# Kernel tuning notes

Hardware: AMD Instinct MI355X
Metric: run time of the kernel (lower is better)

The kernel has to match this reference:

```python
import jax, jax.numpy as jnp
import numpy as np

B, T, D = 64, 2048, 512
UNITS = 10  # hardcoded in original module


def setup_inputs() -> dict:
    key = jax.random.key(0)
    ks = jax.random.split(key, 6)
    Eo = jax.random.normal(ks[0], (B, T, D), dtype=jnp.float32)
    H = jax.random.normal(ks[1], (B, D), dtype=jnp.float32)
    # Keras Dense params: kernel [in, out], bias [out] (glorot-ish scale)
    W_eo = jax.random.normal(ks[2], (D, UNITS), dtype=jnp.float32) * (1.0 / np.sqrt(D))
    b_eo = jnp.zeros((UNITS,), dtype=jnp.float32)
    W_h = jax.random.normal(ks[3], (D, UNITS), dtype=jnp.float32) * (1.0 / np.sqrt(D))
    b_h = jnp.zeros((UNITS,), dtype=jnp.float32)
    W_s = jax.random.normal(ks[4], (UNITS, 1), dtype=jnp.float32) * (1.0 / np.sqrt(UNITS))
    b_s = jnp.zeros((1,), dtype=jnp.float32)
    return {"Eo": Eo, "H": H, "W_eo": W_eo, "b_eo": b_eo,
            "W_h": W_h, "b_h": b_h, "W_s": W_s, "b_s": b_s}


def reference(Eo, H, W_eo, b_eo, W_h, b_h, W_s, b_s):
    # Eo: [B, T, D], H: [B, D]
    Eo_d = jnp.einsum('btd,du->btu', Eo, W_eo) + b_eo          # [B, T, U]
    H_d = H @ W_h + b_h                                        # [B, U]
    EoH = jnp.tanh(Eo_d + H_d[:, None, :])                     # [B, T, U]
    score = jnp.einsum('btu,uo->bto', EoH, W_s) + b_s          # [B, T, 1]
    weight = jax.nn.softmax(score, axis=1)                     # softmax over T
    context = jnp.sum(Eo * weight, axis=1)                     # [B, D]
    return (context, weight)
```

## Files before the change

### kernel.cpp

```cpp
#include <hip/hip_runtime.h>
#include <math.h>

#define BB 64
#define TT 2048
#define DD 512
#define UU 10
#define S_CHUNKS 16
#define CHUNK_T (TT / S_CHUNKS)
#define NB (CHUNK_T / 16)

__device__ __forceinline__ float fast_tanh(float x) {
    return 1.0f - 2.0f / (1.0f + __expf(2.0f * x));
}

template<int K>
__device__ __forceinline__ float dpp_shr(float x) {
    int xi = __builtin_bit_cast(int, x);
    int r  = __builtin_amdgcn_update_dpp(0, xi, 0x110 | K, 0xF, 0xF, true);
    return __builtin_bit_cast(float, r);
}

__device__ __forceinline__ float read_lane_f(float v, int lane) {
    return __builtin_bit_cast(float,
        __builtin_amdgcn_readlane(__builtin_bit_cast(int, v), lane));
}

typedef __attribute__((address_space(1))) const void gvoid;
typedef __attribute__((address_space(3))) void lvoid;
__device__ __forceinline__ void dma16(const float* g, float* l) {
    __builtin_amdgcn_global_load_lds((gvoid*)g, (lvoid*)l, 16, 0, 0);
}

__global__ __launch_bounds__(256) void attn_pass1(
    const float* __restrict__ Eo, const float* __restrict__ H,
    const float* __restrict__ W_eo, const float* __restrict__ b_eo,
    const float* __restrict__ W_h, const float* __restrict__ b_h,
    const float* __restrict__ W_s, const float* __restrict__ b_s,
    float* __restrict__ pexp, float* __restrict__ pc)
{
    const int b     = blockIdx.y;
    const int chunk = blockIdx.x;
    const int tid   = threadIdx.x;
    const int wave  = tid >> 6;
    const int lane  = tid & 63;

    __shared__ __align__(16) float buf[4][2][4][DD];
    __shared__ float sc[4][DD];

    float hacc[UU];
    #pragma unroll
    for (int u = 0; u < UU; ++u) hacc[u] = 0.f;
    const float* Hb = H + (size_t)b * DD;
    #pragma unroll
    for (int k = 0; k < DD / 64; ++k) {
        float hv = Hb[k * 64 + lane];
        const float* wr = W_h + (size_t)(k * 64 + lane) * UU;
        #pragma unroll
        for (int u = 0; u < UU; ++u) hacc[u] += hv * wr[u];
    }
    #pragma unroll
    for (int off = 1; off < 64; off <<= 1) {
        #pragma unroll
        for (int u = 0; u < UU; ++u) hacc[u] += __shfl_xor(hacc[u], off, 64);
    }
    float hb[UU];
    #pragma unroll
    for (int u = 0; u < UU; ++u) hb[u] = hacc[u] + b_h[u] + b_eo[u];

    float wsv[UU];
    #pragma unroll
    for (int u = 0; u < UU; ++u) wsv[u] = W_s[u];
    const float bs = b_s[0];

    float wv[8][UU];
    #pragma unroll
    for (int k = 0; k < 2; ++k) {
        #pragma unroll
        for (int j = 0; j < 4; ++j) {
            const float* wr = W_eo + (size_t)(k * 256 + 4 * lane + j) * UU;
            #pragma unroll
            for (int u = 0; u < UU; ++u) wv[k * 4 + j][u] = wr[u];
        }
    }

    float l = 0.f;
    float c[8];
    #pragma unroll
    for (int j = 0; j < 8; ++j) c[j] = 0.f;

    const int  t0w  = chunk * CHUNK_T + wave * (CHUNK_T / 4);
    const bool lo32 = (lane & 32) == 0;
    const bool lo16 = (lane & 16) == 0;
    const float* rowb = Eo + (size_t)b * TT * DD + 4 * lane;

    #pragma unroll
    for (int tt = 0; tt < 4; ++tt) {
        const float* g = rowb + (size_t)(t0w + tt) * DD;
        dma16(g,       &buf[wave][0][tt][0]);
        dma16(g + 256, &buf[wave][0][tt][256]);
    }

    auto do_batch = [&](int i) {
        const int cur = i & 1, nxt = cur ^ 1;
        if (i + 1 < NB) {
            #pragma unroll
            for (int tt = 0; tt < 4; ++tt) {
                const float* g = rowb + (size_t)(t0w + (i + 1) * 4 + tt) * DD;
                dma16(g,       &buf[wave][nxt][tt][0]);
                dma16(g + 256, &buf[wave][nxt][tt][256]);
            }
        }
        __builtin_amdgcn_sched_barrier(0);

        const int tb = t0w + i * 4;
        float e[4][8];
        #pragma unroll
        for (int tt = 0; tt < 4; ++tt) {
            float4 e0 = *(const float4*)&buf[wave][cur][tt][4 * lane];
            float4 e1 = *(const float4*)&buf[wave][cur][tt][256 + 4 * lane];
            e[tt][0] = e0.x; e[tt][1] = e0.y; e[tt][2] = e0.z; e[tt][3] = e0.w;
            e[tt][4] = e1.x; e[tt][5] = e1.y; e[tt][6] = e1.z; e[tt][7] = e1.w;
        }

        float acc[4][UU];
        #pragma unroll
        for (int tt = 0; tt < 4; ++tt) {
            #pragma unroll
            for (int u = 0; u < UU; ++u) acc[tt][u] = 0.f;
            #pragma unroll
            for (int j = 0; j < 8; ++j) {
                #pragma unroll
                for (int u = 0; u < UU; ++u) acc[tt][u] += e[tt][j] * wv[j][u];
            }
        }

        float s = bs;
        #pragma unroll
        for (int u = 0; u < UU; ++u) {
            float y0 = lo32 ? acc[0][u] : acc[2][u];
            float o0 = lo32 ? acc[2][u] : acc[0][u];
            y0 += __shfl_xor(o0, 32, 64);
            float y1 = lo32 ? acc[1][u] : acc[3][u];
            float o1 = lo32 ? acc[3][u] : acc[1][u];
            y1 += __shfl_xor(o1, 32, 64);
            float z  = lo16 ? y0 : y1;
            float oz = lo16 ? y1 : y0;
            z += __shfl_xor(oz, 16, 64);
            z += dpp_shr<1>(z);
            z += dpp_shr<2>(z);
            z += dpp_shr<4>(z);
            z += dpp_shr<8>(z);
            s += wsv[u] * fast_tanh(z + hb[u]);
        }
        float p = __expf(s);

        if ((lane & 15) == 15) pexp[(size_t)b * TT + tb + (lane >> 4)] = p;

        float p0 = read_lane_f(p, 15);
        float p1 = read_lane_f(p, 31);
        float p2 = read_lane_f(p, 47);
        float p3 = read_lane_f(p, 63);
        l += (p0 + p1) + (p2 + p3);
        #pragma unroll
        for (int j = 0; j < 8; ++j)
            c[j] += p0 * e[0][j] + p1 * e[1][j] + p2 * e[2][j] + p3 * e[3][j];
    };

    asm volatile("s_waitcnt vmcnt(0)" ::: "memory");
    __builtin_amdgcn_sched_barrier(0);
    do_batch(0);
    for (int i = 1; i < NB; ++i) {
        asm volatile("s_waitcnt vmcnt(1)" ::: "memory");
        __builtin_amdgcn_sched_barrier(0);
        do_batch(i);
    }

    #pragma unroll
    for (int k = 0; k < 2; ++k) {
        #pragma unroll
        for (int j = 0; j < 4; ++j)
            sc[wave][k * 256 + 4 * lane + j] = c[k * 4 + j];
    }
    __syncthreads();

    const int pidx = b * S_CHUNKS + chunk;
    for (int d = tid; d < DD; d += 256) {
        pc[(size_t)pidx * DD + d] = (sc[0][d] + sc[1][d]) + (sc[2][d] + sc[3][d]);
    }
}

__global__ __launch_bounds__(256) void attn_epilogue(
    const float* __restrict__ pexp, const float* __restrict__ pc,
    float* __restrict__ ctx_out, float* __restrict__ wout)
{
    const int b    = blockIdx.x >> 2;
    const int part = blockIdx.x & 3;
    const int tid  = threadIdx.x;
    const int wave = tid >> 6;

    float s = 0.f;
    #pragma unroll
    for (int k = 0; k < TT / 256; ++k) s += pexp[(size_t)b * TT + k * 256 + tid];
    #pragma unroll
    for (int off = 1; off < 64; off <<= 1) s += __shfl_xor(s, off, 64);

    __shared__ float sl[4];
    if ((tid & 63) == 0) sl[wave] = s;
    __syncthreads();
    const float l = (sl[0] + sl[1]) + (sl[2] + sl[3]);
    const float inv = 1.0f / l;

    const int d = part * (DD / 4) + tid;
    if (tid < DD / 4) {
        float v = 0.f;
        #pragma unroll
        for (int sss = 0; sss < S_CHUNKS; ++sss)
            v += pc[((size_t)(b * S_CHUNKS + sss)) * DD + d];
        ctx_out[(size_t)b * DD + d] = v * inv;
    }
    #pragma unroll
    for (int k = 0; k < 2; ++k) {
        const int t = part * (TT / 4) + k * 256 + tid;
        wout[(size_t)b * TT + t] = pexp[(size_t)b * TT + t] * inv;
    }
}

extern "C" void kernel_launch(void* const* d_in, const int* in_sizes, int n_in,
                              void* d_out, int out_size, void* d_ws, size_t ws_size,
                              hipStream_t stream) {
    const float* Eo   = (const float*)d_in[0];
    const float* H    = (const float*)d_in[1];
    const float* W_eo = (const float*)d_in[2];
    const float* b_eo = (const float*)d_in[3];
    const float* W_h  = (const float*)d_in[4];
    const float* b_h  = (const float*)d_in[5];
    const float* W_s  = (const float*)d_in[6];
    const float* b_s  = (const float*)d_in[7];

    float* pexp = (float*)d_ws;
    float* pc   = pexp + (size_t)BB * TT;

    float* out_ctx = (float*)d_out;
    float* out_w   = out_ctx + (size_t)BB * DD;

    dim3 gridA(S_CHUNKS, BB);
    attn_pass1<<<gridA, 256, 0, stream>>>(Eo, H, W_eo, b_eo, W_h, b_h, W_s, b_s,
                                          pexp, pc);
    attn_epilogue<<<BB * 4, 256, 0, stream>>>(pexp, pc, out_ctx, out_w);
}
```

Before: 65.32 us.

## Fuse epilogue into main kernel via last-block atomic counter

```diff
diff --git a/kernel.cpp b/kernel.cpp
--- a/kernel.cpp
+++ b/kernel.cpp
@@ -31,12 +31,18 @@
     __builtin_amdgcn_global_load_lds((gvoid*)g, (lvoid*)l, 16, 0, 0);
 }
 
-__global__ __launch_bounds__(256) void attn_pass1(
+__global__ void zero_cnt(int* __restrict__ cnt) {
+    if ((int)threadIdx.x < BB) cnt[threadIdx.x] = 0;
+}
+
+__global__ __launch_bounds__(256) void attn_fused(
     const float* __restrict__ Eo, const float* __restrict__ H,
     const float* __restrict__ W_eo, const float* __restrict__ b_eo,
     const float* __restrict__ W_h, const float* __restrict__ b_h,
     const float* __restrict__ W_s, const float* __restrict__ b_s,
-    float* __restrict__ pexp, float* __restrict__ pc)
+    float* __restrict__ pexp, float* __restrict__ pc,
+    int* __restrict__ cnt,
+    float* __restrict__ ctx_out, float* __restrict__ wout)
 {
     const int b     = blockIdx.y;
     const int chunk = blockIdx.x;
@@ -46,6 +52,8 @@
 
     __shared__ __align__(16) float buf[4][2][4][DD];
     __shared__ float sc[4][DD];
+    __shared__ float sl[4];
+    __shared__ int   s_last;
 
     float hacc[UU];
     #pragma unroll
@@ -187,42 +195,31 @@
     for (int d = tid; d < DD; d += 256) {
         pc[(size_t)pidx * DD + d] = (sc[0][d] + sc[1][d]) + (sc[2][d] + sc[3][d]);
     }
-}
-
-__global__ __launch_bounds__(256) void attn_epilogue(
-    const float* __restrict__ pexp, const float* __restrict__ pc,
-    float* __restrict__ ctx_out, float* __restrict__ wout)
-{
-    const int b    = blockIdx.x >> 2;
-    const int part = blockIdx.x & 3;
-    const int tid  = threadIdx.x;
-    const int wave = tid >> 6;
-
-    float s = 0.f;
-    #pragma unroll
-    for (int k = 0; k < TT / 256; ++k) s += pexp[(size_t)b * TT + k * 256 + tid];
-    #pragma unroll
-    for (int off = 1; off < 64; off <<= 1) s += __shfl_xor(s, off, 64);
-
-    __shared__ float sl[4];
-    if ((tid & 63) == 0) sl[wave] = s;
+
+    __threadfence();
+    if (tid == 0) s_last = (atomicAdd(&cnt[b], 1) == S_CHUNKS - 1);
     __syncthreads();
-    const float l = (sl[0] + sl[1]) + (sl[2] + sl[3]);
-    const float inv = 1.0f / l;
-
-    const int d = part * (DD / 4) + tid;
-    if (tid < DD / 4) {
+    if (!s_last) return;
+    __threadfence();
+
+    float s2 = 0.f;
+    #pragma unroll
+    for (int k = 0; k < TT / 256; ++k) s2 += pexp[(size_t)b * TT + k * 256 + tid];
+    #pragma unroll
+    for (int off = 1; off < 64; off <<= 1) s2 += __shfl_xor(s2, off, 64);
+    if (lane == 0) sl[wave] = s2;
+    __syncthreads();
+    const float linv = 1.0f / ((sl[0] + sl[1]) + (sl[2] + sl[3]));
+
+    for (int d = tid; d < DD; d += 256) {
         float v = 0.f;
         #pragma unroll
-        for (int sss = 0; sss < S_CHUNKS; ++sss)
-            v += pc[((size_t)(b * S_CHUNKS + sss)) * DD + d];
-        ctx_out[(size_t)b * DD + d] = v * inv;
-    }
-    #pragma unroll
-    for (int k = 0; k < 2; ++k) {
-        const int t = part * (TT / 4) + k * 256 + tid;
-        wout[(size_t)b * TT + t] = pexp[(size_t)b * TT + t] * inv;
-    }
+        for (int ss = 0; ss < S_CHUNKS; ++ss)
+            v += pc[((size_t)(b * S_CHUNKS + ss)) * DD + d];
+        ctx_out[(size_t)b * DD + d] = v * linv;
+    }
+    for (int t = tid; t < TT; t += 256)
+        wout[(size_t)b * TT + t] = pexp[(size_t)b * TT + t] * linv;
 }
 
 extern "C" void kernel_launch(void* const* d_in, const int* in_sizes, int n_in,
@@ -239,12 +236,13 @@
 
     float* pexp = (float*)d_ws;
     float* pc   = pexp + (size_t)BB * TT;
+    int*   cnt  = (int*)(pc + (size_t)BB * S_CHUNKS * DD);
 
     float* out_ctx = (float*)d_out;
     float* out_w   = out_ctx + (size_t)BB * DD;
 
+    zero_cnt<<<1, 64, 0, stream>>>(cnt);
     dim3 gridA(S_CHUNKS, BB);
-    attn_pass1<<<gridA, 256, 0, stream>>>(Eo, H, W_eo, b_eo, W_h, b_h, W_s, b_s,
-                                          pexp, pc);
-    attn_epilogue<<<BB * 4, 256, 0, stream>>>(pexp, pc, out_ctx, out_w);
-}
+    attn_fused<<<gridA, 256, 0, stream>>>(Eo, H, W_eo, b_eo, W_h, b_h, W_s, b_s,
+                                          pexp, pc, cnt, out_ctx, out_w);
+}
```

New measurement: 227.4 us. +248.1%, slower.
